# Kernel optimization log

Hardware: AMD Instinct MI355X
Metric: run time of the kernel (lower is better)

Reference implementation:

```python
import jax, jax.numpy as jnp
import numpy as np

B, C, H, W = 2, 256, 64, 64
HEADS = 4


def _conv1x1(x, w, b):
    # x: [B,C,H,W], w: [O,C], b: [O] -> [B,O,H,W]
    return jnp.einsum('bchw,oc->bohw', x, w) + b[None, :, None, None]


def setup_inputs() -> dict:
    key = jax.random.key(0)
    ks = jax.random.split(key, 10)
    s = 1.0 / np.sqrt(C)
    inp = {
        'input_tensor1': jax.random.normal(ks[0], (B, C, H, W), jnp.float32),
        'input_tensor2': jax.random.normal(ks[1], (B, C, H, W), jnp.float32),
        'W1': jax.random.normal(ks[2], (C, C), jnp.float32) * s,
        'b1': jax.random.normal(ks[3], (C,), jnp.float32) * 0.01,
        'W2': jax.random.normal(ks[4], (C, C), jnp.float32) * s,
        'b2': jax.random.normal(ks[5], (C,), jnp.float32) * 0.01,
        'W3': jax.random.normal(ks[6], (C, C), jnp.float32) * s,
        'b3': jax.random.normal(ks[7], (C,), jnp.float32) * 0.01,
        'W4': jax.random.normal(ks[8], (C, C), jnp.float32) * s,
        'b4': jax.random.normal(ks[9], (C,), jnp.float32) * 0.01,
    }
    return inp


def reference(input_tensor1, input_tensor2, W1, b1, W2, b2, W3, b3, W4, b4):
    b_, c_, h_, w_ = input_tensor2.shape
    n = h_ * w_
    d = c_ // HEADS  # channels per head block (raw reshape, mixes channel/spatial)
    bh = b_ * HEADS
    # faithful torch .view of contiguous [B,C,H,W] -> (B*headn, H*W, C//headn)
    self_k = _conv1x1(input_tensor1, W1, b1).reshape(bh, n, d)
    self_q = _conv1x1(input_tensor1, W2, b2).reshape(bh, n, d).transpose(0, 2, 1)
    self_v = _conv1x1(input_tensor2, W3, b3).reshape(bh, n, d)
    kq = jnp.matmul(self_k, self_q)                 # [bh, n, n]
    # GLOBAL softmax over the fully flattened n*n scores per batch-head
    kqs = jax.nn.softmax(kq.reshape(bh, n * n), axis=-1).reshape(bh, n, n)
    kqv = jnp.matmul(kqs, self_v)                   # [bh, n, d]
    kqv = kqv.reshape(b_, c_, h_, w_)
    return _conv1x1(kqv, W4, b4)
```

## Files before the change

### kernel.cpp

```cpp
#include <hip/hip_runtime.h>
#include <math.h>

#define CC 256
#define NSP 4096
#define L2E 1.44269504088896340736f
#define SH2 (48.0f * L2E)

typedef float f32x4  __attribute__((ext_vector_type(4)));
typedef float f32x16 __attribute__((ext_vector_type(16)));
typedef _Float16 half8 __attribute__((ext_vector_type(8)));
typedef short short8 __attribute__((ext_vector_type(8)));
typedef unsigned short u16;
typedef unsigned int   u32;

__device__ __forceinline__ u16 bf16rne(float x) {
    unsigned u = __float_as_uint(x);
    u += 0x7FFFu + ((u >> 16) & 1u);
    return (u16)(u >> 16);
}
__device__ __forceinline__ half8 ld_frag(const u16* p) {
    int4 v = *(const int4*)p;
    return __builtin_bit_cast(half8, v);
}
__device__ __forceinline__ short8 ld_bfrag(const u16* p) {
    int4 v = *(const int4*)p;
    return __builtin_bit_cast(short8, v);
}
__device__ __forceinline__ u32 pkrtz(float a, float b) {
    return __builtin_bit_cast(u32, __builtin_amdgcn_cvt_pkrtz(a, b));
}
__device__ __forceinline__ u16 f16b(float x) {
    _Float16 h = (_Float16)x;
    return __builtin_bit_cast(u16, h);
}
__device__ __forceinline__ float f16f(u16 v) {
    return (float)__builtin_bit_cast(_Float16, v);
}

__global__ __launch_bounds__(256) void wpack(
    const float* __restrict__ W1, const float* __restrict__ W2,
    const float* __restrict__ W3, const float* __restrict__ W4,
    u16* __restrict__ Whi, u16* __restrict__ Wlo)
{
    const int slot = blockIdx.y;
    const float* W = slot == 0 ? W1 : slot == 1 ? W2 : slot == 2 ? W3 : W4;
    const int i = (blockIdx.x * 256 + threadIdx.x) * 4;
    const int o = i >> 8, c0 = i & 255;
    const f32x4 v = *(const f32x4*)(W + i);
    ushort4 h4, l4;
    h4.x = bf16rne(v.x); l4.x = bf16rne(v.x - __uint_as_float((u32)h4.x << 16));
    h4.y = bf16rne(v.y); l4.y = bf16rne(v.y - __uint_as_float((u32)h4.y << 16));
    h4.z = bf16rne(v.z); l4.z = bf16rne(v.z - __uint_as_float((u32)h4.z << 16));
    h4.w = bf16rne(v.w); l4.w = bf16rne(v.w - __uint_as_float((u32)h4.w << 16));
    const int fi = ((c0 >> 3) * 256 + o) * 8 + (c0 & 7);
    *(ushort4*)(Whi + slot * 65536 + fi) = h4;
    *(ushort4*)(Wlo + slot * 65536 + fi) = l4;
}

__global__ __launch_bounds__(256) void conv_qkv(
    const float* __restrict__ in1, const float* __restrict__ in2,
    const u16* __restrict__ Wpk_hi, const u16* __restrict__ Wpk_lo,
    const float* __restrict__ b1, const float* __restrict__ b2,
    const float* __restrict__ b3,
    u16* __restrict__ Khi, u16* __restrict__ Klo,
    u16* __restrict__ Qpk, u16* __restrict__ Vpk)
{
    __shared__ __align__(16) u16 Xhi[32 * 256];
    __shared__ __align__(16) u16 Xlo[32 * 256];

    const int tid = threadIdx.x;
    const int w = tid >> 6, l = tid & 63;
    const int h = l >> 5, ln = l & 31;
    const int st = blockIdx.x;
    const int proj = blockIdx.y;
    const int b = blockIdx.z;
    const int s0 = st * 32;

    const float* x = (proj == 2) ? in2 : in1;
    const u16* Wh = Wpk_hi + proj * 65536;
    const u16* Wl = Wpk_lo + proj * 65536;
    const float* bias = proj == 0 ? b1 : proj == 1 ? b2 : b3;

#pragma unroll
    for (int i = 0; i < 4; ++i) {
        const int c0 = w * 64 + (h * 4 + i) * 8;
        float xv[8];
#pragma unroll
        for (int cc = 0; cc < 8; ++cc)
            xv[cc] = x[((size_t)b * CC + c0 + cc) * NSP + s0 + ln];
        u32 hw[4], lw[4];
#pragma unroll
        for (int p2 = 0; p2 < 4; ++p2) {
            const u16 h0 = bf16rne(xv[2 * p2]);
            const u16 h1 = bf16rne(xv[2 * p2 + 1]);
            const u16 l0 = bf16rne(xv[2 * p2]     - __uint_as_float((u32)h0 << 16));
            const u16 l1 = bf16rne(xv[2 * p2 + 1] - __uint_as_float((u32)h1 << 16));
            hw[p2] = (u32)h0 | ((u32)h1 << 16);
            lw[p2] = (u32)l0 | ((u32)l1 << 16);
        }
        const int off = ((ln * 256 + c0) * 2) ^ ((ln & 7) << 4);
        *(uint4*)((char*)Xhi + off) = make_uint4(hw[0], hw[1], hw[2], hw[3]);
        *(uint4*)((char*)Xlo + off) = make_uint4(lw[0], lw[1], lw[2], lw[3]);
    }
    __syncthreads();

    f32x16 acc[2];
#pragma unroll
    for (int ti = 0; ti < 2; ++ti)
#pragma unroll
        for (int i = 0; i < 16; ++i) acc[ti][i] = 0.f;

#pragma unroll 2
    for (int kk = 0; kk < 16; ++kk) {
        const int kc = kk * 16 + h * 8;
        short8 ah[2], al[2];
#pragma unroll
        for (int ti = 0; ti < 2; ++ti) {
            const size_t fi = ((size_t)(kc >> 3) * 256 + w * 64 + ti * 32 + ln) * 8;
            ah[ti] = ld_bfrag(Wh + fi);
            al[ti] = ld_bfrag(Wl + fi);
        }
        const int off = ((ln * 256 + kc) * 2) ^ ((ln & 7) << 4);
        const short8 bh_ = *(const short8*)((const char*)Xhi + off);
        const short8 bl_ = *(const short8*)((const char*)Xlo + off);
#pragma unroll
        for (int ti = 0; ti < 2; ++ti) {
            acc[ti] = __builtin_amdgcn_mfma_f32_32x32x16_bf16(ah[ti], bh_, acc[ti], 0, 0, 0);
            acc[ti] = __builtin_amdgcn_mfma_f32_32x32x16_bf16(ah[ti], bl_, acc[ti], 0, 0, 0);
            acc[ti] = __builtin_amdgcn_mfma_f32_32x32x16_bf16(al[ti], bh_, acc[ti], 0, 0, 0);
        }
    }

    const int sg = s0 + ln;
#pragma unroll
    for (int ti = 0; ti < 2; ++ti)
#pragma unroll
        for (int reg = 0; reg < 16; ++reg) {
            const int o = w * 64 + ti * 32 + (reg & 3) + 8 * (reg >> 2) + 4 * h;
            const size_t SLB = (size_t)((b * 4 + (o >> 6)) * 64 + (o & 63)) * 4096;
            const float av0 = acc[ti][reg] + bias[o];
            if (proj == 2) {
                const size_t ui = SLB + (size_t)((sg >> 9) * 64 + (sg & 63)) * 8 + ((sg >> 6) & 7);
                Vpk[ui] = f16b(av0);
            } else {
                const float av = (proj == 0) ? av0 * L2E : av0;
                const _Float16 hf = (_Float16)av;
                const size_t ui = SLB + (size_t)(((sg >> 3) & 7) * 64 + (sg >> 6)) * 8 + (sg & 7);
                if (proj == 0) {
                    Khi[ui] = __builtin_bit_cast(u16, hf);
                    Klo[ui] = f16b(av - (float)hf);
                } else {
                    Qpk[ui] = __builtin_bit_cast(u16, hf);
                }
            }
        }
}

__global__ __launch_bounds__(256, 2) void flash3(
    const u16* __restrict__ Khi, const u16* __restrict__ Klo,
    const u16* __restrict__ Qpk, const u16* __restrict__ Vpk,
    u16* __restrict__ Oparth, float* __restrict__ zpart)
{
    const int tid = threadIdx.x;
    const int w = tid >> 6, l = tid & 63;
    const int h = l >> 5, ln = l & 31;
    const int id = blockIdx.x;
    const int bh = id & 7, qq = (id >> 3) & 7, tb = id >> 6;
    const int b = bh >> 2, hd = bh & 3;
    const int t = tb * 4 + w;

    const u16* Kh = Khi + (size_t)(bh * 64 + t) * 4096;
    const u16* Kl = Klo + (size_t)(bh * 64 + t) * 4096;

    half8 kf_h[2][4], kf_l[2][4];
#pragma unroll
    for (int rt = 0; rt < 2; ++rt)
#pragma unroll
        for (int ks = 0; ks < 4; ++ks) {
            const int cix = ((ks * 2 + h) * 64 + rt * 32 + ln) * 8;
            kf_h[rt][ks] = ld_frag(Kh + cix);
            kf_l[rt][ks] = ld_frag(Kl + cix);
        }

    f32x16 oacc[2][2];
#pragma unroll
    for (int rt = 0; rt < 2; ++rt)
#pragma unroll
        for (int ft = 0; ft < 2; ++ft)
#pragma unroll
            for (int i = 0; i < 16; ++i) oacc[rt][ft][i] = 0.f;
    float zacc[2] = {0.f, 0.f};

    for (int it = 0; it < 8; ++it) {
        const int tq = qq * 8 + it;
        const u16* Qt = Qpk + (size_t)(bh * 64 + tq) * 4096;
        const u16* Vt = Vpk + (size_t)(bh * 64 + tq) * 4096;
#pragma unroll
        for (int jt = 0; jt < 2; ++jt) {
            half8 qf[4];
#pragma unroll
            for (int ks = 0; ks < 4; ++ks)
                qf[ks] = ld_frag(Qt + ((ks * 2 + h) * 64 + jt * 32 + ln) * 8);

            f32x16 sa[2];
#pragma unroll
            for (int rt = 0; rt < 2; ++rt)
#pragma unroll
                for (int i = 0; i < 16; ++i) sa[rt][i] = -SH2;
            __builtin_amdgcn_s_setprio(1);
#pragma unroll
            for (int ks = 0; ks < 4; ++ks) {
                sa[0] = __builtin_amdgcn_mfma_f32_32x32x16_f16(qf[ks], kf_h[0][ks], sa[0], 0, 0, 0);
                sa[1] = __builtin_amdgcn_mfma_f32_32x32x16_f16(qf[ks], kf_h[1][ks], sa[1], 0, 0, 0);
                sa[0] = __builtin_amdgcn_mfma_f32_32x32x16_f16(qf[ks], kf_l[0][ks], sa[0], 0, 0, 0);
                sa[1] = __builtin_amdgcn_mfma_f32_32x32x16_f16(qf[ks], kf_l[1][ks], sa[1], 0, 0, 0);
            }
            __builtin_amdgcn_s_setprio(0);

            half8 vf[2][2];
#pragma unroll
            for (int js = 0; js < 2; ++js)
#pragma unroll
                for (int ft = 0; ft < 2; ++ft)
                    vf[js][ft] = ld_frag(Vt + (((jt * 2 + js) * 2 + h) * 64 + ft * 32 + ln) * 8);

#pragma unroll
            for (int rt = 0; rt < 2; ++rt) {
                float p[16]; float zs = 0.f;
#pragma unroll
                for (int i = 0; i < 16; ++i) {
                    p[i] = __builtin_amdgcn_exp2f(sa[rt][i]);
                    zs += p[i];
                }
                zacc[rt] += zs;
                u32 wd[8], sw[8];
#pragma unroll
                for (int i = 0; i < 8; ++i) wd[i] = pkrtz(p[2 * i], p[2 * i + 1]);
#pragma unroll
                for (int i = 0; i < 8; ++i) sw[i] = (u32)__shfl_xor((int)wd[i], 32);
                int4 c0 = make_int4((int)(h ? sw[2] : wd[0]), (int)(h ? sw[3] : wd[1]),
                                    (int)(h ? wd[2] : sw[0]), (int)(h ? wd[3] : sw[1]));
                int4 c1 = make_int4((int)(h ? sw[6] : wd[4]), (int)(h ? sw[7] : wd[5]),
                                    (int)(h ? wd[6] : sw[4]), (int)(h ? wd[7] : sw[5]));
                const half8 pf0 = __builtin_bit_cast(half8, c0);
                const half8 pf1 = __builtin_bit_cast(half8, c1);
                __builtin_amdgcn_s_setprio(1);
                oacc[rt][0] = __builtin_amdgcn_mfma_f32_32x32x16_f16(pf0, vf[0][0], oacc[rt][0], 0, 0, 0);
                oacc[rt][0] = __builtin_amdgcn_mfma_f32_32x32x16_f16(pf1, vf[1][0], oacc[rt][0], 0, 0, 0);
                oacc[rt][1] = __builtin_amdgcn_mfma_f32_32x32x16_f16(pf0, vf[0][1], oacc[rt][1], 0, 0, 0);
                oacc[rt][1] = __builtin_amdgcn_mfma_f32_32x32x16_f16(pf1, vf[1][1], oacc[rt][1], 0, 0, 0);
                __builtin_amdgcn_s_setprio(0);
            }
        }
    }

#pragma unroll
    for (int rt = 0; rt < 2; ++rt) {
        const float z2 = zacc[rt] + __shfl_xor(zacc[rt], 32);
        if (h == 0)
            zpart[((size_t)qq * 8 + bh) * NSP + t * 64 + rt * 32 + ln] = z2;
    }
    const size_t ob = ((size_t)(qq * 2 + b) * CC + hd * 64 + t) * NSP;
#pragma unroll
    for (int rt = 0; rt < 2; ++rt)
#pragma unroll
        for (int ft = 0; ft < 2; ++ft)
#pragma unroll
            for (int reg = 0; reg < 16; ++reg) {
                const int rin = (reg & 3) + 8 * (reg >> 2) + 4 * h;
                Oparth[ob + (size_t)(rt * 32 + rin) * 64 + ft * 32 + ln]
                    = f16b(oacc[rt][ft][reg]);
            }
}

__global__ __launch_bounds__(256) void reduce_kernel(
    const float* __restrict__ zp, float* __restrict__ coef)
{
    __shared__ float red[256];
    const int tid = threadIdx.x, bh = blockIdx.x;
    float lz = 0.f;
    for (int i = tid; i < 8 * NSP; i += 256) {
        const int qq = i >> 12, r = i & 4095;
        lz += zp[((size_t)qq * 8 + bh) * NSP + r];
    }
    red[tid] = lz; __syncthreads();
    for (int s = 128; s > 0; s >>= 1) {
        if (tid < s) red[tid] += red[tid + s];
        __syncthreads();
    }
    if (tid == 0) coef[bh] = 1.f / red[0];
}

__global__ __launch_bounds__(256) void conv_out(
    const u16* __restrict__ Oparth,
    const u16* __restrict__ Wpk_hi, const u16* __restrict__ Wpk_lo,
    const float* __restrict__ b4, const float* __restrict__ coef,
    float* __restrict__ out)
{
    __shared__ __align__(16) u16 Xhi[32 * 256];
    __shared__ __align__(16) u16 Xlo[32 * 256];

    const int tid = threadIdx.x;
    const int w = tid >> 6, l = tid & 63;
    const int h = l >> 5, ln = l & 31;
    const int st = blockIdx.x;
    const int oh = blockIdx.y;
    const int b = blockIdx.z;
    const int s0 = st * 32;

    const u16* Wh = Wpk_hi + 3 * 65536;
    const u16* Wl = Wpk_lo + 3 * 65536;
    const size_t TENu = (size_t)2 * CC * NSP;

    const float cf = coef[b * 4 + w];
#pragma unroll
    for (int i = 0; i < 4; ++i) {
        const int c0 = w * 64 + (h * 4 + i) * 8;
        float xv[8];
#pragma unroll
        for (int cc = 0; cc < 8; ++cc) {
            const size_t base = ((size_t)b * CC + c0 + cc) * NSP + s0 + ln;
            float s = 0.f;
#pragma unroll
            for (int pp = 0; pp < 8; ++pp)
                s += f16f(Oparth[pp * TENu + base]);
            xv[cc] = s * cf;
        }
        u32 hw[4], lw[4];
#pragma unroll
        for (int p2 = 0; p2 < 4; ++p2) {
            const u16 h0 = bf16rne(xv[2 * p2]);
            const u16 h1 = bf16rne(xv[2 * p2 + 1]);
            const u16 l0 = bf16rne(xv[2 * p2]     - __uint_as_float((u32)h0 << 16));
            const u16 l1 = bf16rne(xv[2 * p2 + 1] - __uint_as_float((u32)h1 << 16));
            hw[p2] = (u32)h0 | ((u32)h1 << 16);
            lw[p2] = (u32)l0 | ((u32)l1 << 16);
        }
        const int off = ((ln * 256 + c0) * 2) ^ ((ln & 7) << 4);
        *(uint4*)((char*)Xhi + off) = make_uint4(hw[0], hw[1], hw[2], hw[3]);
        *(uint4*)((char*)Xlo + off) = make_uint4(lw[0], lw[1], lw[2], lw[3]);
    }
    __syncthreads();

    f32x16 acc;
#pragma unroll
    for (int i = 0; i < 16; ++i) acc[i] = 0.f;

#pragma unroll 2
    for (int kk = 0; kk < 16; ++kk) {
        const int kc = kk * 16 + h * 8;
        const size_t fi = ((size_t)(kc >> 3) * 256 + oh * 128 + w * 32 + ln) * 8;
        const short8 ah = ld_bfrag(Wh + fi);
        const short8 al = ld_bfrag(Wl + fi);
        const int off = ((ln * 256 + kc) * 2) ^ ((ln & 7) << 4);
        const short8 bh_ = *(const short8*)((const char*)Xhi + off);
        const short8 bl_ = *(const short8*)((const char*)Xlo + off);
        acc = __builtin_amdgcn_mfma_f32_32x32x16_bf16(ah, bh_, acc, 0, 0, 0);
        acc = __builtin_amdgcn_mfma_f32_32x32x16_bf16(ah, bl_, acc, 0, 0, 0);
        acc = __builtin_amdgcn_mfma_f32_32x32x16_bf16(al, bh_, acc, 0, 0, 0);
    }

    const int sg = s0 + ln;
#pragma unroll
    for (int reg = 0; reg < 16; ++reg) {
        const int o = oh * 128 + w * 32 + (reg & 3) + 8 * (reg >> 2) + 4 * h;
        out[((size_t)b * CC + o) * NSP + sg] = acc[reg] + b4[o];
    }
}

extern "C" void kernel_launch(void* const* d_in, const int* in_sizes, int n_in,
                              void* d_out, int out_size, void* d_ws, size_t ws_size,
                              hipStream_t stream)
{
    (void)in_sizes; (void)n_in; (void)out_size; (void)ws_size;
    const float* in1 = (const float*)d_in[0];
    const float* in2 = (const float*)d_in[1];
    const float* W1 = (const float*)d_in[2]; const float* b1 = (const float*)d_in[3];
    const float* W2 = (const float*)d_in[4]; const float* b2 = (const float*)d_in[5];
    const float* W3 = (const float*)d_in[6]; const float* b3 = (const float*)d_in[7];
    const float* W4 = (const float*)d_in[8]; const float* b4 = (const float*)d_in[9];
    float* out = (float*)d_out;

    const size_t TEN = (size_t)2 * CC * NSP;
    char* p = (char*)d_ws;
    u16* Khi = (u16*)p; p += TEN * 2;
    u16* Klo = (u16*)p; p += TEN * 2;
    u16* Qpk = (u16*)p; p += TEN * 2;
    u16* Vpk = (u16*)p; p += TEN * 2;
    u16* Wph = (u16*)p; p += 4 * 65536 * 2;
    u16* Wpl = (u16*)p; p += 4 * 65536 * 2;
    u16* Oparth = (u16*)p; p += 8 * TEN * 2;
    float* zpart = (float*)p; p += (size_t)8 * 8 * NSP * 4;
    float* coef  = (float*)p;

    wpack<<<dim3(64, 4), 256, 0, stream>>>(W1, W2, W3, W4, Wph, Wpl);
    conv_qkv<<<dim3(128, 3, 2), 256, 0, stream>>>(
        in1, in2, Wph, Wpl, b1, b2, b3, Khi, Klo, Qpk, Vpk);
    flash3<<<dim3(1024), 256, 0, stream>>>(Khi, Klo, Qpk, Vpk, Oparth, zpart);
    reduce_kernel<<<dim3(8), 256, 0, stream>>>(zpart, coef);
    conv_out<<<dim3(128, 2, 2), 256, 0, stream>>>(Oparth, Wph, Wpl, b4, coef, out);
}
```

Before: 146.1 us.

## Drop split-fp16 K and reduce partial outputs in shared memory

The K projection is now stored as a single fp16 value instead of a hi/lo pair, which halves the score MFMAs and the K loads in the attention kernel. The attention kernel's work split is rearranged so each block's four waves handle different query chunks against the same K tile. Their output accumulators are summed in shared memory through serialized turns and written as two fp32 partials instead of eight fp16 partials. This cuts global write and read traffic for the partial outputs and the summation work in conv_out. The cost is lower precision in the global-softmax scores and extra LDS traffic plus four barriers per block.

```diff
diff --git a/kernel.cpp b/kernel.cpp
--- a/kernel.cpp
+++ b/kernel.cpp
@@ -32,9 +32,6 @@
 __device__ __forceinline__ u16 f16b(float x) {
     _Float16 h = (_Float16)x;
     return __builtin_bit_cast(u16, h);
-}
-__device__ __forceinline__ float f16f(u16 v) {
-    return (float)__builtin_bit_cast(_Float16, v);
 }
 
 __global__ __launch_bounds__(256) void wpack(
@@ -62,8 +59,7 @@
     const u16* __restrict__ Wpk_hi, const u16* __restrict__ Wpk_lo,
     const float* __restrict__ b1, const float* __restrict__ b2,
     const float* __restrict__ b3,
-    u16* __restrict__ Khi, u16* __restrict__ Klo,
-    u16* __restrict__ Qpk, u16* __restrict__ Vpk)
+    u16* __restrict__ Kpk, u16* __restrict__ Qpk, u16* __restrict__ Vpk)
 {
     __shared__ __align__(16) u16 Xhi[32 * 256];
     __shared__ __align__(16) u16 Xlo[32 * 256];
@@ -144,43 +140,36 @@
                 Vpk[ui] = f16b(av0);
             } else {
                 const float av = (proj == 0) ? av0 * L2E : av0;
-                const _Float16 hf = (_Float16)av;
                 const size_t ui = SLB + (size_t)(((sg >> 3) & 7) * 64 + (sg >> 6)) * 8 + (sg & 7);
-                if (proj == 0) {
-                    Khi[ui] = __builtin_bit_cast(u16, hf);
-                    Klo[ui] = f16b(av - (float)hf);
-                } else {
-                    Qpk[ui] = __builtin_bit_cast(u16, hf);
-                }
+                u16* dst = (proj == 0) ? Kpk : Qpk;
+                dst[ui] = f16b(av);
             }
         }
 }
 
 __global__ __launch_bounds__(256, 2) void flash3(
-    const u16* __restrict__ Khi, const u16* __restrict__ Klo,
-    const u16* __restrict__ Qpk, const u16* __restrict__ Vpk,
-    u16* __restrict__ Oparth, float* __restrict__ zpart)
-{
+    const u16* __restrict__ Kpk, const u16* __restrict__ Qpk,
+    const u16* __restrict__ Vpk,
+    float* __restrict__ Opf, float* __restrict__ zpart)
+{
+    __shared__ float Osum[64 * 64];
+
     const int tid = threadIdx.x;
     const int w = tid >> 6, l = tid & 63;
     const int h = l >> 5, ln = l & 31;
     const int id = blockIdx.x;
-    const int bh = id & 7, qq = (id >> 3) & 7, tb = id >> 6;
+    const int bh = id & 7, half = (id >> 3) & 1, t = id >> 4;
     const int b = bh >> 2, hd = bh & 3;
-    const int t = tb * 4 + w;
-
-    const u16* Kh = Khi + (size_t)(bh * 64 + t) * 4096;
-    const u16* Kl = Klo + (size_t)(bh * 64 + t) * 4096;
-
-    half8 kf_h[2][4], kf_l[2][4];
+    const int qq = half * 4 + w;
+
+    const u16* Kh = Kpk + (size_t)(bh * 64 + t) * 4096;
+
+    half8 kf[2][4];
 #pragma unroll
     for (int rt = 0; rt < 2; ++rt)
 #pragma unroll
-        for (int ks = 0; ks < 4; ++ks) {
-            const int cix = ((ks * 2 + h) * 64 + rt * 32 + ln) * 8;
-            kf_h[rt][ks] = ld_frag(Kh + cix);
-            kf_l[rt][ks] = ld_frag(Kl + cix);
-        }
+        for (int ks = 0; ks < 4; ++ks)
+            kf[rt][ks] = ld_frag(Kh + ((ks * 2 + h) * 64 + rt * 32 + ln) * 8);
 
     f32x16 oacc[2][2];
 #pragma unroll
@@ -210,10 +199,8 @@
             __builtin_amdgcn_s_setprio(1);
 #pragma unroll
             for (int ks = 0; ks < 4; ++ks) {
-                sa[0] = __builtin_amdgcn_mfma_f32_32x32x16_f16(qf[ks], kf_h[0][ks], sa[0], 0, 0, 0);
-                sa[1] = __builtin_amdgcn_mfma_f32_32x32x16_f16(qf[ks], kf_h[1][ks], sa[1], 0, 0, 0);
-                sa[0] = __builtin_amdgcn_mfma_f32_32x32x16_f16(qf[ks], kf_l[0][ks], sa[0], 0, 0, 0);
-                sa[1] = __builtin_amdgcn_mfma_f32_32x32x16_f16(qf[ks], kf_l[1][ks], sa[1], 0, 0, 0);
+                sa[0] = __builtin_amdgcn_mfma_f32_32x32x16_f16(qf[ks], kf[0][ks], sa[0], 0, 0, 0);
+                sa[1] = __builtin_amdgcn_mfma_f32_32x32x16_f16(qf[ks], kf[1][ks], sa[1], 0, 0, 0);
             }
             __builtin_amdgcn_s_setprio(0);
 
@@ -260,17 +247,30 @@
         if (h == 0)
             zpart[((size_t)qq * 8 + bh) * NSP + t * 64 + rt * 32 + ln] = z2;
     }
-    const size_t ob = ((size_t)(qq * 2 + b) * CC + hd * 64 + t) * NSP;
-#pragma unroll
-    for (int rt = 0; rt < 2; ++rt)
-#pragma unroll
-        for (int ft = 0; ft < 2; ++ft)
-#pragma unroll
-            for (int reg = 0; reg < 16; ++reg) {
-                const int rin = (reg & 3) + 8 * (reg >> 2) + 4 * h;
-                Oparth[ob + (size_t)(rt * 32 + rin) * 64 + ft * 32 + ln]
-                    = f16b(oacc[rt][ft][reg]);
-            }
+
+    for (int turn = 0; turn < 4; ++turn) {
+        if (w == turn) {
+#pragma unroll
+            for (int rt = 0; rt < 2; ++rt)
+#pragma unroll
+                for (int ft = 0; ft < 2; ++ft)
+#pragma unroll
+                    for (int reg = 0; reg < 16; ++reg) {
+                        const int row = rt * 32 + (reg & 3) + 8 * (reg >> 2) + 4 * h;
+                        const int col = ft * 32 + ln;
+                        if (turn == 0) Osum[row * 64 + col] = oacc[rt][ft][reg];
+                        else           Osum[row * 64 + col] += oacc[rt][ft][reg];
+                    }
+        }
+        __syncthreads();
+    }
+    float* Od = Opf + (size_t)half * ((size_t)2 * CC * NSP)
+              + ((size_t)(b * CC + hd * 64 + t)) * NSP;
+#pragma unroll
+    for (int i = 0; i < 4; ++i) {
+        const int idx = tid + 256 * i;
+        *(f32x4*)(Od + idx * 4) = *(const f32x4*)(Osum + idx * 4);
+    }
 }
 
 __global__ __launch_bounds__(256) void reduce_kernel(
@@ -292,7 +292,7 @@
 }
 
 __global__ __launch_bounds__(256) void conv_out(
-    const u16* __restrict__ Oparth,
+    const float* __restrict__ Opf,
     const u16* __restrict__ Wpk_hi, const u16* __restrict__ Wpk_lo,
     const float* __restrict__ b4, const float* __restrict__ coef,
     float* __restrict__ out)
@@ -310,7 +310,7 @@
 
     const u16* Wh = Wpk_hi + 3 * 65536;
     const u16* Wl = Wpk_lo + 3 * 65536;
-    const size_t TENu = (size_t)2 * CC * NSP;
+    const size_t TENf = (size_t)2 * CC * NSP;
 
     const float cf = coef[b * 4 + w];
 #pragma unroll
@@ -320,11 +320,7 @@
 #pragma unroll
         for (int cc = 0; cc < 8; ++cc) {
             const size_t base = ((size_t)b * CC + c0 + cc) * NSP + s0 + ln;
-            float s = 0.f;
-#pragma unroll
-            for (int pp = 0; pp < 8; ++pp)
-                s += f16f(Oparth[pp * TENu + base]);
-            xv[cc] = s * cf;
+            xv[cc] = (Opf[base] + Opf[TENf + base]) * cf;
         }
         u32 hw[4], lw[4];
 #pragma unroll
@@ -383,20 +379,19 @@
 
     const size_t TEN = (size_t)2 * CC * NSP;
     char* p = (char*)d_ws;
-    u16* Khi = (u16*)p; p += TEN * 2;
-    u16* Klo = (u16*)p; p += TEN * 2;
+    u16* Kpk = (u16*)p; p += TEN * 2;
     u16* Qpk = (u16*)p; p += TEN * 2;
     u16* Vpk = (u16*)p; p += TEN * 2;
     u16* Wph = (u16*)p; p += 4 * 65536 * 2;
     u16* Wpl = (u16*)p; p += 4 * 65536 * 2;
-    u16* Oparth = (u16*)p; p += 8 * TEN * 2;
+    float* Opf = (float*)p; p += 2 * TEN * 4;
     float* zpart = (float*)p; p += (size_t)8 * 8 * NSP * 4;
     float* coef  = (float*)p;
 
     wpack<<<dim3(64, 4), 256, 0, stream>>>(W1, W2, W3, W4, Wph, Wpl);
     conv_qkv<<<dim3(128, 3, 2), 256, 0, stream>>>(
-        in1, in2, Wph, Wpl, b1, b2, b3, Khi, Klo, Qpk, Vpk);
-    flash3<<<dim3(1024), 256, 0, stream>>>(Khi, Klo, Qpk, Vpk, Oparth, zpart);
+        in1, in2, Wph, Wpl, b1, b2, b3, Kpk, Qpk, Vpk);
+    flash3<<<dim3(1024), 256, 0, stream>>>(Kpk, Qpk, Vpk, Opf, zpart);
     reduce_kernel<<<dim3(8), 256, 0, stream>>>(zpart, coef);
-    conv_out<<<dim3(128, 2, 2), 256, 0, stream>>>(Oparth, Wph, Wpl, b4, coef, out);
-}
+    conv_out<<<dim3(128, 2, 2), 256, 0, stream>>>(Opf, Wph, Wpl, b4, coef, out);
+}
```

Result: faster. 126.7 us (-13.3%).
